# Kernel optimization log

Measured on AMD Instinct MI355X. Metric: run time of the kernel, lower is better.

## Reference

```python
import jax, jax.numpy as jnp
import numpy as np

N = 50000      # nodes
E = 800000     # edges (avg degree 16)
F = 32         # n_features
FOUT = 32      # n_features_out
L = 2          # n_layers (Message+Update pairs)
LEN = 10.0     # length_scale


def _mlp(x, w1, b1, w2, b2):
    # embedding.MLP: Linear -> SiLU -> Linear
    return jax.nn.silu(x @ w1 + b1) @ w2 + b2


def _posenc(d):
    # sinusoidal PositionalEncoder(F, length=LEN): ranks 1..F/2
    ranks = jnp.arange(1, F // 2 + 1, dtype=d.dtype)
    a = d[:, None] * ranks * (jnp.pi / LEN)           # [E, F/2]
    return jnp.concatenate([jnp.sin(a), jnp.cos(a)], axis=-1)  # [E, F]


def _painn(s, v, edge_index, edge_dist, edge_dir,
           mp_w1, mp_b1, mp_w2, mp_b2, mw_w1, mw_b1, mw_w2, mw_b2,
           u_U, u_V, u_w1, u_b1, u_w2, u_b2,
           ro_w1, ro_b1, ro_w2, ro_b2, ro_V):
    src, dst = edge_index[0], edge_index[1]
    pe = _posenc(edge_dist)                            # [E, F]
    dirb = edge_dir[:, None, :]                        # [E, 1, 3]
    for l in range(L):
        # ---- Message ----
        mix = _mlp(s[src], mp_w1[l], mp_b1[l], mp_w2[l], mp_b2[l]) \
            * _mlp(pe, mw_w1[l], mw_b1[l], mw_w2[l], mw_b2[l])     # [E, 4F]
        gates, cpg, sed, sf = jnp.split(mix, 4, axis=-1)
        cross = jnp.cross(dirb, v[dst])                # [E, F, 3] (broadcast)
        dv = sed[:, :, None] * dirb + gates[:, :, None] * v[src] \
           + cpg[:, :, None] * cross                   # [E, F, 3]
        ds = sf * s[src]                               # [E, F]
        v = v + jax.ops.segment_sum(dv, dst, num_segments=N)
        s = s + jax.ops.segment_sum(ds, dst, num_segments=N)
        # ---- Update ----
        Vv = jnp.einsum('nfc,fg->ngc', v, u_V[l])      # [N, F, 3]
        Uv = jnp.einsum('nfc,fg->ngc', v, u_U[l])
        Vn = jnp.linalg.norm(Vv, axis=-1)              # [N, F]
        g, ssn, add = jnp.split(
            _mlp(jnp.concatenate([Vn, s], axis=-1), u_w1[l], u_b1[l], u_w2[l], u_b2[l]),
            3, axis=-1)
        v = v + g[:, :, None] * Uv
        s = s + Vn * Vn * ssn + add
    # ---- Readout ----
    inv_out, gates = jnp.split(_mlp(s, ro_w1, ro_b1, ro_w2, ro_b2), 2, axis=-1)
    eqv_out = gates[:, :, None] * jnp.einsum('nfc,fg->ngc', v, ro_V)
    return inv_out, eqv_out


def setup_inputs() -> dict:
    key = jax.random.key(0)
    ks = iter(jax.random.split(key, 64))
    nk = lambda: next(ks)
    lin = lambda fin, fout, *lead: (jax.random.normal(nk(), (*lead, fin, fout), jnp.float32)
                                    / np.sqrt(fin).astype(np.float32))
    d = {}
    d['invariant_node_features'] = jax.random.normal(nk(), (N, F), jnp.float32)
    d['equivariant_node_features'] = jax.random.normal(nk(), (N, F, 3), jnp.float32)
    d['edge_index'] = jax.random.randint(nk(), (2, E), 0, N)
    d['edge_dist'] = jax.random.uniform(nk(), (E,), jnp.float32) * LEN
    g = jax.random.normal(nk(), (E, 3), jnp.float32)
    d['edge_dir'] = g / jnp.linalg.norm(g, axis=-1, keepdims=True)
    # Message MLPs (phi on node features, W on positional encoding)
    d['mp_w1'] = lin(F, F, L); d['mp_b1'] = jnp.zeros((L, F), jnp.float32)
    d['mp_w2'] = lin(F, 4 * F, L); d['mp_b2'] = jnp.zeros((L, 4 * F), jnp.float32)
    d['mw_w1'] = lin(F, F, L); d['mw_b1'] = jnp.zeros((L, F), jnp.float32)
    d['mw_w2'] = lin(F, 4 * F, L); d['mw_b2'] = jnp.zeros((L, 4 * F), jnp.float32)
    # Update: EquivariantLinear U, V and MLP(2F -> F -> 3F)
    d['u_U'] = lin(F, F, L); d['u_V'] = lin(F, F, L)
    d['u_w1'] = lin(2 * F, F, L); d['u_b1'] = jnp.zeros((L, F), jnp.float32)
    d['u_w2'] = lin(F, 3 * F, L); d['u_b2'] = jnp.zeros((L, 3 * F), jnp.float32)
    # Readout: MLP(F -> F -> 2*FOUT) and EquivariantLinear V (F -> FOUT)
    d['ro_w1'] = lin(F, F); d['ro_b1'] = jnp.zeros((F,), jnp.float32)
    d['ro_w2'] = lin(F, 2 * FOUT); d['ro_b2'] = jnp.zeros((2 * FOUT,), jnp.float32)
    d['ro_V'] = lin(F, FOUT)
    return d


def reference(invariant_node_features, equivariant_node_features, edge_index,
              edge_dist, edge_dir,
              mp_w1, mp_b1, mp_w2, mp_b2, mw_w1, mw_b1, mw_w2, mw_b2,
              u_U, u_V, u_w1, u_b1, u_w2, u_b2,
              ro_w1, ro_b1, ro_w2, ro_b2, ro_V):
    return _painn(invariant_node_features, equivariant_node_features, edge_index,
                  edge_dist, edge_dir,
                  mp_w1, mp_b1, mp_w2, mp_b2, mw_w1, mw_b1, mw_w2, mw_b2,
                  u_U, u_V, u_w1, u_b1, u_w2, u_b2,
                  ro_w1, ro_b1, ro_w2, ro_b2, ro_V)
```

## Files before the change

### kernel.cpp

```cpp
#include <hip/hip_runtime.h>
#include <math.h>

#define PI_LEN 0.3141592653589793f
#define LEN_F  10.0f
#define TBL    4096

__device__ __forceinline__ float fsilu(float x) {
  return x * __builtin_amdgcn_rcpf(1.f + __expf(-x));
}

__global__ __launch_bounds__(256) void hist_kernel(const int* __restrict__ ei,
                                                   int* __restrict__ deg, int E_) {
  int e = blockIdx.x * 256 + threadIdx.x;
  if (e < E_) atomicAdd(&deg[ei[E_ + e]], 1);
}

__global__ __launch_bounds__(1024) void scan_kernel(const int* __restrict__ deg,
                                                    int* __restrict__ off,
                                                    int* __restrict__ cursor, int N_) {
  __shared__ int wtot[16];
  __shared__ int carry_s;
  int tid = threadIdx.x, lane = tid & 63, wid = tid >> 6;
  if (tid == 0) carry_s = 0;
  __syncthreads();
  int nch = (N_ + 8191) / 8192;
  for (int c = 0; c < nch; ++c) {
    int base_idx = c * 8192 + tid * 8;
    int x[8]; int mysum = 0;
    #pragma unroll
    for (int j = 0; j < 8; ++j) { int idx = base_idx + j; x[j] = (idx < N_) ? deg[idx] : 0; mysum += x[j]; }
    int incl = mysum;
    #pragma unroll
    for (int s = 1; s < 64; s <<= 1) { int t = __shfl_up(incl, s, 64); if (lane >= s) incl += t; }
    if (lane == 63) wtot[wid] = incl;
    __syncthreads();
    if (wid == 0) {
      int wt = (lane < 16) ? wtot[lane] : 0;
      #pragma unroll
      for (int s = 1; s < 16; s <<= 1) { int t = __shfl_up(wt, s, 64); if (lane >= s) wt += t; }
      if (lane < 16) wtot[lane] = wt;
    }
    __syncthreads();
    int wexcl = (wid > 0) ? wtot[wid - 1] : 0;
    int run = carry_s + wexcl + (incl - mysum);
    #pragma unroll
    for (int j = 0; j < 8; ++j) {
      int idx = base_idx + j;
      if (idx < N_) { off[idx] = run; cursor[idx] = run; }
      run += x[j];
    }
    __syncthreads();
    if (tid == 0) carry_s += wtot[15];
    __syncthreads();
  }
  if (tid == 0) off[N_] = carry_s;
}

__global__ __launch_bounds__(256) void scatter_kernel(
    const int* __restrict__ ei, const float* __restrict__ dist,
    const float* __restrict__ edir, int* __restrict__ cursor,
    int* __restrict__ srcp, float4* __restrict__ edata, int E_) {
  int e = blockIdx.x * 256 + threadIdx.x;
  if (e < E_) {
    int dst = ei[E_ + e];
    int pos = atomicAdd(&cursor[dst], 1);
    srcp[pos] = ei[e];
    edata[pos] = make_float4(edir[3*e], edir[3*e+1], edir[3*e+2], dist[e]);
  }
}

__global__ __launch_bounds__(256) void nodeA_kernel(
    const float* __restrict__ s, const float* __restrict__ w1,
    const float* __restrict__ b1, const float* __restrict__ w2,
    const float* __restrict__ b2, float4* __restrict__ Aout4, int N_)
{
  __shared__ float xld[8][32];
  __shared__ float hld[8][32];
  int tid = threadIdx.x, i = tid >> 5, g = tid & 31;
  long n = (long)blockIdx.x * 8 + i;
  bool ok = (n < N_);
  xld[i][g] = ok ? s[n*32 + g] : 0.f;
  __syncthreads();
  float acc = b1[g];
  for (int k = 0; k < 32; ++k) acc += xld[i][k] * w1[k*32 + g];
  hld[i][g] = fsilu(acc);
  __syncthreads();
  float o0 = b2[g], o1 = b2[32+g], o2 = b2[64+g], o3 = b2[96+g];
  for (int k = 0; k < 32; ++k) {
    float hk = hld[i][k];
    o0 += hk * w2[k*128 +      g];
    o1 += hk * w2[k*128 + 32 + g];
    o2 += hk * w2[k*128 + 64 + g];
    o3 += hk * w2[k*128 + 96 + g];
  }
  if (ok) Aout4[n*32 + g] = make_float4(o0, o1, o2, o3 * xld[i][g]);
}

__global__ __launch_bounds__(256) void tbl_kernel(
    const float* __restrict__ w1, const float* __restrict__ b1,
    const float* __restrict__ w2, const float* __restrict__ b2,
    float4* __restrict__ tbl4)
{
  __shared__ float peld[8][32];
  __shared__ float hld[8][32];
  int tid = threadIdx.x, i = tid >> 5, g = tid & 31;
  int t = blockIdx.x * 8 + i;
  bool okt = (t <= TBL);
  float d = (float)t * (LEN_F / (float)TBL);
  float pe = (g < 16) ? __sinf(d * (float)(g + 1) * PI_LEN)
                      : __cosf(d * (float)(g - 15) * PI_LEN);
  peld[i][g] = pe;
  __syncthreads();
  float h = b1[g];
  for (int k = 0; k < 32; ++k) h += peld[i][k] * w1[k*32 + g];
  hld[i][g] = fsilu(h);
  __syncthreads();
  float o0 = b2[g], o1 = b2[32+g], o2 = b2[64+g], o3 = b2[96+g];
  for (int k = 0; k < 32; ++k) {
    float hk = hld[i][k];
    o0 += hk * w2[k*128 +      g];
    o1 += hk * w2[k*128 + 32 + g];
    o2 += hk * w2[k*128 + 64 + g];
    o3 += hk * w2[k*128 + 96 + g];
  }
  if (okt) tbl4[(long)t*32 + g] = make_float4(o0, o1, o2, o3);
}

#define EDGE_MATH(ED, M0, M1, FR, Av, V0, V1, V2)                         \
  {                                                                        \
    float ga = M0.x + FR*(M1.x - M0.x);                                    \
    float ca = M0.y + FR*(M1.y - M0.y);                                    \
    float da = M0.z + FR*(M1.z - M0.z);                                    \
    float sa = M0.w + FR*(M1.w - M0.w);                                    \
    float gates = ga*Av.x, cpg = ca*Av.y, sed = da*Av.z;                   \
    acc_s += sa*Av.w;                                                      \
    float crx = ED.y*vd2 - ED.z*vd1;                                       \
    float cry = ED.z*vd0 - ED.x*vd2;                                       \
    float crz = ED.x*vd1 - ED.y*vd0;                                       \
    av0 += sed*ED.x + gates*V0 + cpg*crx;                                  \
    av1 += sed*ED.y + gates*V1 + cpg*cry;                                  \
    av2 += sed*ED.z + gates*V2 + cpg*crz;                                  \
  }

__global__ __launch_bounds__(256) void gather_kernel(
    const int* __restrict__ off, const int* __restrict__ srcp,
    const float4* __restrict__ edata, const float4* __restrict__ tbl4,
    const float* __restrict__ v_prev, const float4* __restrict__ Aout4,
    float4* __restrict__ acc4, int N_)
{
  int tid = threadIdx.x, w = tid >> 6, lane = tid & 63, g = lane & 31, hf = lane >> 5;
  int n = blockIdx.x * 4 + w;
  if (n >= N_) return;
  const float* vp = v_prev + (long)n*96 + g*3;
  float vd0 = vp[0], vd1 = vp[1], vd2 = vp[2];
  int pstart = off[n], pend = off[n + 1];
  float acc_s = 0, av0 = 0, av1 = 0, av2 = 0;
  const float inv_step = (float)TBL / LEN_F;

  int deg = pend - pstart;
  int nfull = deg >> 3;
  int pb = pstart + hf * 4;
  for (int it = 0; it < nfull; ++it, pb += 8) {
    int srcs[4]; float4 ed[4];
    #pragma unroll
    for (int b = 0; b < 4; ++b) { srcs[b] = srcp[pb + b]; ed[b] = edata[pb + b]; }
    float4 m0[4], m1[4], A[4]; float fr[4];
    float vs0[4], vs1[4], vs2[4];
    #pragma unroll
    for (int b = 0; b < 4; ++b) {
      float x = ed[b].w * inv_step;
      float f = floorf(x);
      int i0 = (int)f; if (i0 > TBL - 1) i0 = TBL - 1;
      fr[b] = x - f;
      m0[b] = tbl4[(long)i0*32 + g];
      m1[b] = tbl4[(long)(i0 + 1)*32 + g];
      A[b]  = Aout4[(long)srcs[b]*32 + g];
      const float* vq = v_prev + (long)srcs[b]*96 + g*3;
      vs0[b] = vq[0]; vs1[b] = vq[1]; vs2[b] = vq[2];
    }
    #pragma unroll
    for (int b = 0; b < 4; ++b)
      EDGE_MATH(ed[b], m0[b], m1[b], fr[b], A[b], vs0[b], vs1[b], vs2[b]);
  }
  int p = pstart + nfull * 8 + hf;
  for (; p + 2 < pend; p += 4) {
    int  s0_ = srcp[p], s1_ = srcp[p + 2];
    float4 e0 = edata[p], e1 = edata[p + 2];
    float x0 = e0.w * inv_step, x1 = e1.w * inv_step;
    float f0 = floorf(x0), f1 = floorf(x1);
    int i0 = (int)f0; if (i0 > TBL - 1) i0 = TBL - 1;
    int i1 = (int)f1; if (i1 > TBL - 1) i1 = TBL - 1;
    float r0 = x0 - f0, r1 = x1 - f1;
    float4 a0 = tbl4[(long)i0*32 + g], b0 = tbl4[(long)(i0+1)*32 + g];
    float4 a1 = tbl4[(long)i1*32 + g], b1 = tbl4[(long)(i1+1)*32 + g];
    float4 A0 = Aout4[(long)s0_*32 + g], A1 = Aout4[(long)s1_*32 + g];
    const float* vq0 = v_prev + (long)s0_*96 + g*3;
    const float* vq1 = v_prev + (long)s1_*96 + g*3;
    float u0 = vq0[0], u1 = vq0[1], u2 = vq0[2];
    float t0 = vq1[0], t1 = vq1[1], t2 = vq1[2];
    EDGE_MATH(e0, a0, b0, r0, A0, u0, u1, u2);
    EDGE_MATH(e1, a1, b1, r1, A1, t0, t1, t2);
  }
  if (p < pend) {
    int  s0_ = srcp[p];
    float4 e0 = edata[p];
    float x0 = e0.w * inv_step;
    float f0 = floorf(x0);
    int i0 = (int)f0; if (i0 > TBL - 1) i0 = TBL - 1;
    float r0 = x0 - f0;
    float4 a0 = tbl4[(long)i0*32 + g], b0 = tbl4[(long)(i0+1)*32 + g];
    float4 A0 = Aout4[(long)s0_*32 + g];
    const float* vq0 = v_prev + (long)s0_*96 + g*3;
    float u0 = vq0[0], u1 = vq0[1], u2 = vq0[2];
    EDGE_MATH(e0, a0, b0, r0, A0, u0, u1, u2);
  }
  av0   += __shfl_xor(av0, 32);
  av1   += __shfl_xor(av1, 32);
  av2   += __shfl_xor(av2, 32);
  acc_s += __shfl_xor(acc_s, 32);
  if (hf == 0) acc4[(long)n*32 + g] = make_float4(av0, av1, av2, acc_s);
}

__global__ __launch_bounds__(256) void update_kernel(
    const float* __restrict__ s_prev, const float* __restrict__ v_prev,
    const float4* __restrict__ acc4,
    const float* __restrict__ uU, const float* __restrict__ uV,
    const float* __restrict__ uw1, const float* __restrict__ ub1,
    const float* __restrict__ uw2, const float* __restrict__ ub2,
    float* __restrict__ s_out, float* __restrict__ v_out, int N_)
{
  __shared__ float vld[8][96];
  __shared__ float in64[8][64];
  __shared__ float hld[8][32];
  int tid = threadIdx.x, i = tid >> 5, g = tid & 31;
  long n = (long)blockIdx.x * 8 + i;
  bool ok = (n < N_);
  float nv0 = 0, nv1 = 0, nv2 = 0, ns = 0;
  if (ok) {
    float4 a = acc4[n*32 + g];
    const float* vp = v_prev + n*96 + g*3;
    nv0 = vp[0] + a.x; nv1 = vp[1] + a.y; nv2 = vp[2] + a.z;
    ns  = s_prev[n*32 + g] + a.w;
  }
  vld[i][g*3+0] = nv0; vld[i][g*3+1] = nv1; vld[i][g*3+2] = nv2;
  __syncthreads();
  float Vv0=0,Vv1=0,Vv2=0,Uv0=0,Uv1=0,Uv2=0;
  for (int f = 0; f < 32; ++f) {
    float wu = uU[f*32 + g];
    float wv = uV[f*32 + g];
    float v0 = vld[i][f*3+0], v1 = vld[i][f*3+1], v2 = vld[i][f*3+2];
    Vv0 += v0*wv; Vv1 += v1*wv; Vv2 += v2*wv;
    Uv0 += v0*wu; Uv1 += v1*wu; Uv2 += v2*wu;
  }
  float Vn = sqrtf(Vv0*Vv0 + Vv1*Vv1 + Vv2*Vv2);
  in64[i][g] = Vn; in64[i][32 + g] = ns;
  __syncthreads();
  float h = ub1[g];
  for (int k = 0; k < 64; ++k) h += in64[i][k] * uw1[k*32 + g];
  h = fsilu(h);
  hld[i][g] = h;
  __syncthreads();
  float og = ub2[g], ossn = ub2[32 + g], oadd = ub2[64 + g];
  for (int k = 0; k < 32; ++k) {
    float hk = hld[i][k];
    og   += hk * uw2[k*96 +      g];
    ossn += hk * uw2[k*96 + 32 + g];
    oadd += hk * uw2[k*96 + 64 + g];
  }
  if (ok) {
    float* vo = v_out + n*96 + g*3;
    vo[0] = nv0 + og*Uv0;
    vo[1] = nv1 + og*Uv1;
    vo[2] = nv2 + og*Uv2;
    s_out[n*32 + g] = ns + Vn*Vn*ossn + oadd;
  }
}

__global__ __launch_bounds__(256) void readout_kernel(
    const float* __restrict__ s_cur, const float* __restrict__ v_cur,
    const float* __restrict__ w1, const float* __restrict__ b1,
    const float* __restrict__ w2, const float* __restrict__ b2,
    const float* __restrict__ roV, float* __restrict__ out, int N_)
{
  __shared__ float sld[8][32];
  __shared__ float hld[8][32];
  __shared__ float vld[8][96];
  int tid = threadIdx.x, i = tid >> 5, g = tid & 31;
  long n = (long)blockIdx.x * 8 + i;
  bool ok = (n < N_);
  if (ok) {
    sld[i][g] = s_cur[n*32 + g];
    const float* vp = v_cur + n*96 + g*3;
    vld[i][g*3+0] = vp[0]; vld[i][g*3+1] = vp[1]; vld[i][g*3+2] = vp[2];
  } else {
    sld[i][g] = 0.f;
    vld[i][g*3+0] = vld[i][g*3+1] = vld[i][g*3+2] = 0.f;
  }
  __syncthreads();
  float h = b1[g];
  for (int k = 0; k < 32; ++k) h += sld[i][k] * w1[k*32 + g];
  h = fsilu(h);
  hld[i][g] = h;
  __syncthreads();
  float inv = b2[g], gate = b2[32+g];
  for (int k = 0; k < 32; ++k) {
    float hk = hld[i][k];
    inv  += hk * w2[k*64 +      g];
    gate += hk * w2[k*64 + 32 + g];
  }
  float R0=0, R1=0, R2=0;
  for (int f = 0; f < 32; ++f) {
    float wv = roV[f*32 + g];
    R0 += vld[i][f*3+0]*wv; R1 += vld[i][f*3+1]*wv; R2 += vld[i][f*3+2]*wv;
  }
  if (ok) {
    out[n*32 + g] = inv;
    long eb = (long)N_*32 + n*96 + (long)g*3;
    out[eb+0] = gate*R0; out[eb+1] = gate*R1; out[eb+2] = gate*R2;
  }
}

extern "C" void kernel_launch(void* const* d_in, const int* in_sizes, int n_in,
                              void* d_out, int out_size, void* d_ws, size_t ws_size,
                              hipStream_t stream)
{
  const float* s_in  = (const float*)d_in[0];
  const float* v_in  = (const float*)d_in[1];
  const int*   ei    = (const int*)  d_in[2];
  const float* dist  = (const float*)d_in[3];
  const float* edir  = (const float*)d_in[4];
  const float* mp_w1 = (const float*)d_in[5];
  const float* mp_b1 = (const float*)d_in[6];
  const float* mp_w2 = (const float*)d_in[7];
  const float* mp_b2 = (const float*)d_in[8];
  const float* mw_w1 = (const float*)d_in[9];
  const float* mw_b1 = (const float*)d_in[10];
  const float* mw_w2 = (const float*)d_in[11];
  const float* mw_b2 = (const float*)d_in[12];
  const float* u_U   = (const float*)d_in[13];
  const float* u_V   = (const float*)d_in[14];
  const float* u_w1  = (const float*)d_in[15];
  const float* u_b1  = (const float*)d_in[16];
  const float* u_w2  = (const float*)d_in[17];
  const float* u_b2  = (const float*)d_in[18];
  const float* ro_w1 = (const float*)d_in[19];
  const float* ro_b1 = (const float*)d_in[20];
  const float* ro_w2 = (const float*)d_in[21];
  const float* ro_b2 = (const float*)d_in[22];
  const float* ro_V  = (const float*)d_in[23];

  int N_ = in_sizes[0] / 32;
  int E_ = in_sizes[3];

  float*  sA    = (float*)d_ws;
  float*  vA    = sA + (size_t)N_*32;
  float*  sB    = vA + (size_t)N_*96;
  float*  vB    = sB + (size_t)N_*32;
  float4* Aout4 = (float4*)(vB + (size_t)N_*96);
  float4* tbl4  = Aout4 + (size_t)N_*32;
  float4* edata = tbl4 + (size_t)(TBL+1)*32;
  int*    srcp  = (int*)(edata + (size_t)E_);
  int*    deg   = srcp + E_;
  int*    off   = deg + N_;
  int*    cursor= off + N_ + 1;

  float4* acc4  = (float4*)d_out;

  int nodeBlocks  = (N_ + 7) / 8;
  int gathBlocks  = (N_ + 3) / 4;
  int edgeBlocks  = (E_ + 255) / 256;
  int tblBlocks   = (TBL + 1 + 7) / 8;

  hipMemsetAsync(deg, 0, (size_t)N_ * sizeof(int), stream);
  hist_kernel<<<edgeBlocks, 256, 0, stream>>>(ei, deg, E_);
  scan_kernel<<<1, 1024, 0, stream>>>(deg, off, cursor, N_);
  scatter_kernel<<<edgeBlocks, 256, 0, stream>>>(ei, dist, edir, cursor, srcp, edata, E_);

  const float* s_cur = s_in;  const float* v_cur = v_in;
  float* s_nxt = sB;  float* v_nxt = vB;
  for (int l = 0; l < 2; ++l) {
    nodeA_kernel<<<nodeBlocks, 256, 0, stream>>>(
        s_cur, mp_w1 + l*1024, mp_b1 + l*32, mp_w2 + l*4096, mp_b2 + l*128, Aout4, N_);
    tbl_kernel<<<tblBlocks, 256, 0, stream>>>(
        mw_w1 + l*1024, mw_b1 + l*32, mw_w2 + l*4096, mw_b2 + l*128, tbl4);
    gather_kernel<<<gathBlocks, 256, 0, stream>>>(
        off, srcp, edata, tbl4, v_cur, Aout4, acc4, N_);
    update_kernel<<<nodeBlocks, 256, 0, stream>>>(
        s_cur, v_cur, acc4,
        u_U + l*1024, u_V + l*1024, u_w1 + l*2048, u_b1 + l*32,
        u_w2 + l*3072, u_b2 + l*96,
        s_nxt, v_nxt, N_);
    s_cur = s_nxt; v_cur = v_nxt;
    s_nxt = sA;    v_nxt = vA;
  }

  readout_kernel<<<nodeBlocks, 256, 0, stream>>>(
      s_cur, v_cur, ro_w1, ro_b1, ro_w2, ro_b2, ro_V, (float*)d_out, N_);
}
```

Before: 688.9 us.

## Fuse node MLP, table build, update and readout stages; widen masked gather loop

```diff
diff --git a/kernel.cpp b/kernel.cpp
--- a/kernel.cpp
+++ b/kernel.cpp
@@ -69,69 +69,70 @@
   }
 }
 
-__global__ __launch_bounds__(256) void nodeA_kernel(
-    const float* __restrict__ s, const float* __restrict__ w1,
-    const float* __restrict__ b1, const float* __restrict__ w2,
-    const float* __restrict__ b2, float4* __restrict__ Aout4, int N_)
-{
-  __shared__ float xld[8][32];
-  __shared__ float hld[8][32];
-  int tid = threadIdx.x, i = tid >> 5, g = tid & 31;
-  long n = (long)blockIdx.x * 8 + i;
-  bool ok = (n < N_);
-  xld[i][g] = ok ? s[n*32 + g] : 0.f;
-  __syncthreads();
-  float acc = b1[g];
-  for (int k = 0; k < 32; ++k) acc += xld[i][k] * w1[k*32 + g];
-  hld[i][g] = fsilu(acc);
-  __syncthreads();
+__device__ __forceinline__ void mlp_tbl_block(
+    int i, int g, int t,
+    const float* __restrict__ w1, const float* __restrict__ b1,
+    const float* __restrict__ w2, const float* __restrict__ b2,
+    float4* __restrict__ tbl4, float (*pe)[96], float (*hl)[32])
+{
+  bool okt = (t <= TBL);
+  float d = (float)t * (LEN_F / (float)TBL);
+  pe[i][g] = (g < 16) ? __sinf(d * (float)(g + 1) * PI_LEN)
+                      : __cosf(d * (float)(g - 15) * PI_LEN);
+  float h = b1[g];
+  for (int k = 0; k < 32; ++k) h += pe[i][k] * w1[k*32 + g];
+  hl[i][g] = fsilu(h);
   float o0 = b2[g], o1 = b2[32+g], o2 = b2[64+g], o3 = b2[96+g];
   for (int k = 0; k < 32; ++k) {
-    float hk = hld[i][k];
+    float hk = hl[i][k];
     o0 += hk * w2[k*128 +      g];
     o1 += hk * w2[k*128 + 32 + g];
     o2 += hk * w2[k*128 + 64 + g];
     o3 += hk * w2[k*128 + 96 + g];
   }
-  if (ok) Aout4[n*32 + g] = make_float4(o0, o1, o2, o3 * xld[i][g]);
-}
-
-__global__ __launch_bounds__(256) void tbl_kernel(
-    const float* __restrict__ w1, const float* __restrict__ b1,
-    const float* __restrict__ w2, const float* __restrict__ b2,
-    float4* __restrict__ tbl4)
-{
-  __shared__ float peld[8][32];
-  __shared__ float hld[8][32];
+  if (okt) tbl4[(long)t*32 + g] = make_float4(o0, o1, o2, o3);
+}
+
+__global__ __launch_bounds__(256) void nodeA_tbl_kernel(
+    const float* __restrict__ s,
+    const float* __restrict__ mpw1, const float* __restrict__ mpb1,
+    const float* __restrict__ mpw2, const float* __restrict__ mpb2,
+    const float* __restrict__ mww1, const float* __restrict__ mwb1,
+    const float* __restrict__ mww2, const float* __restrict__ mwb2,
+    float4* __restrict__ Aout4, float4* __restrict__ tbl4,
+    int N_, int nodeBlocks)
+{
+  __shared__ float a[8][96];
+  __shared__ float c[8][32];
   int tid = threadIdx.x, i = tid >> 5, g = tid & 31;
-  int t = blockIdx.x * 8 + i;
-  bool okt = (t <= TBL);
-  float d = (float)t * (LEN_F / (float)TBL);
-  float pe = (g < 16) ? __sinf(d * (float)(g + 1) * PI_LEN)
-                      : __cosf(d * (float)(g - 15) * PI_LEN);
-  peld[i][g] = pe;
-  __syncthreads();
-  float h = b1[g];
-  for (int k = 0; k < 32; ++k) h += peld[i][k] * w1[k*32 + g];
-  hld[i][g] = fsilu(h);
-  __syncthreads();
-  float o0 = b2[g], o1 = b2[32+g], o2 = b2[64+g], o3 = b2[96+g];
-  for (int k = 0; k < 32; ++k) {
-    float hk = hld[i][k];
-    o0 += hk * w2[k*128 +      g];
-    o1 += hk * w2[k*128 + 32 + g];
-    o2 += hk * w2[k*128 + 64 + g];
-    o3 += hk * w2[k*128 + 96 + g];
-  }
-  if (okt) tbl4[(long)t*32 + g] = make_float4(o0, o1, o2, o3);
-}
-
-#define EDGE_MATH(ED, M0, M1, FR, Av, V0, V1, V2)                         \
+  if (blockIdx.x >= nodeBlocks) {
+    int t = (blockIdx.x - nodeBlocks) * 8 + i;
+    mlp_tbl_block(i, g, t, mww1, mwb1, mww2, mwb2, tbl4, a, c);
+    return;
+  }
+  long n = (long)blockIdx.x * 8 + i;
+  bool ok = (n < N_);
+  a[i][g] = ok ? s[n*32 + g] : 0.f;
+  float h = mpb1[g];
+  for (int k = 0; k < 32; ++k) h += a[i][k] * mpw1[k*32 + g];
+  c[i][g] = fsilu(h);
+  float o0 = mpb2[g], o1 = mpb2[32+g], o2 = mpb2[64+g], o3 = mpb2[96+g];
+  for (int k = 0; k < 32; ++k) {
+    float hk = c[i][k];
+    o0 += hk * mpw2[k*128 +      g];
+    o1 += hk * mpw2[k*128 + 32 + g];
+    o2 += hk * mpw2[k*128 + 64 + g];
+    o3 += hk * mpw2[k*128 + 96 + g];
+  }
+  if (ok) Aout4[n*32 + g] = make_float4(o0, o1, o2, o3 * a[i][g]);
+}
+
+#define EDGE_MATH_M(ED, M0, M1, FR, MS, Av, V0, V1, V2)                    \
   {                                                                        \
-    float ga = M0.x + FR*(M1.x - M0.x);                                    \
-    float ca = M0.y + FR*(M1.y - M0.y);                                    \
-    float da = M0.z + FR*(M1.z - M0.z);                                    \
-    float sa = M0.w + FR*(M1.w - M0.w);                                    \
+    float ga = (M0.x + FR*(M1.x - M0.x)) * MS;                             \
+    float ca = (M0.y + FR*(M1.y - M0.y)) * MS;                             \
+    float da = (M0.z + FR*(M1.z - M0.z)) * MS;                             \
+    float sa = (M0.w + FR*(M1.w - M0.w)) * MS;                             \
     float gates = ga*Av.x, cpg = ca*Av.y, sed = da*Av.z;                   \
     acc_s += sa*Av.w;                                                      \
     float crx = ED.y*vd2 - ED.z*vd1;                                       \
@@ -157,62 +158,34 @@
   float acc_s = 0, av0 = 0, av1 = 0, av2 = 0;
   const float inv_step = (float)TBL / LEN_F;
 
-  int deg = pend - pstart;
-  int nfull = deg >> 3;
-  int pb = pstart + hf * 4;
-  for (int it = 0; it < nfull; ++it, pb += 8) {
-    int srcs[4]; float4 ed[4];
-    #pragma unroll
-    for (int b = 0; b < 4; ++b) { srcs[b] = srcp[pb + b]; ed[b] = edata[pb + b]; }
-    float4 m0[4], m1[4], A[4]; float fr[4];
-    float vs0[4], vs1[4], vs2[4];
-    #pragma unroll
-    for (int b = 0; b < 4; ++b) {
+  for (int p0 = pstart + hf * 8; p0 < pend; p0 += 16) {
+    int cnt = pend - p0; if (cnt > 8) cnt = 8;
+    int idx[8]; float4 ed[8];
+    #pragma unroll
+    for (int b = 0; b < 8; ++b) {
+      int p = (b < cnt) ? p0 + b : p0;
+      idx[b] = srcp[p];
+      ed[b]  = edata[p];
+    }
+    float4 m0[8], m1[8], A[8]; float fr[8];
+    float vs0[8], vs1[8], vs2[8];
+    #pragma unroll
+    for (int b = 0; b < 8; ++b) {
       float x = ed[b].w * inv_step;
       float f = floorf(x);
       int i0 = (int)f; if (i0 > TBL - 1) i0 = TBL - 1;
       fr[b] = x - f;
       m0[b] = tbl4[(long)i0*32 + g];
       m1[b] = tbl4[(long)(i0 + 1)*32 + g];
-      A[b]  = Aout4[(long)srcs[b]*32 + g];
-      const float* vq = v_prev + (long)srcs[b]*96 + g*3;
+      A[b]  = Aout4[(long)idx[b]*32 + g];
+      const float* vq = v_prev + (long)idx[b]*96 + g*3;
       vs0[b] = vq[0]; vs1[b] = vq[1]; vs2[b] = vq[2];
     }
     #pragma unroll
-    for (int b = 0; b < 4; ++b)
-      EDGE_MATH(ed[b], m0[b], m1[b], fr[b], A[b], vs0[b], vs1[b], vs2[b]);
-  }
-  int p = pstart + nfull * 8 + hf;
-  for (; p + 2 < pend; p += 4) {
-    int  s0_ = srcp[p], s1_ = srcp[p + 2];
-    float4 e0 = edata[p], e1 = edata[p + 2];
-    float x0 = e0.w * inv_step, x1 = e1.w * inv_step;
-    float f0 = floorf(x0), f1 = floorf(x1);
-    int i0 = (int)f0; if (i0 > TBL - 1) i0 = TBL - 1;
-    int i1 = (int)f1; if (i1 > TBL - 1) i1 = TBL - 1;
-    float r0 = x0 - f0, r1 = x1 - f1;
-    float4 a0 = tbl4[(long)i0*32 + g], b0 = tbl4[(long)(i0+1)*32 + g];
-    float4 a1 = tbl4[(long)i1*32 + g], b1 = tbl4[(long)(i1+1)*32 + g];
-    float4 A0 = Aout4[(long)s0_*32 + g], A1 = Aout4[(long)s1_*32 + g];
-    const float* vq0 = v_prev + (long)s0_*96 + g*3;
-    const float* vq1 = v_prev + (long)s1_*96 + g*3;
-    float u0 = vq0[0], u1 = vq0[1], u2 = vq0[2];
-    float t0 = vq1[0], t1 = vq1[1], t2 = vq1[2];
-    EDGE_MATH(e0, a0, b0, r0, A0, u0, u1, u2);
-    EDGE_MATH(e1, a1, b1, r1, A1, t0, t1, t2);
-  }
-  if (p < pend) {
-    int  s0_ = srcp[p];
-    float4 e0 = edata[p];
-    float x0 = e0.w * inv_step;
-    float f0 = floorf(x0);
-    int i0 = (int)f0; if (i0 > TBL - 1) i0 = TBL - 1;
-    float r0 = x0 - f0;
-    float4 a0 = tbl4[(long)i0*32 + g], b0 = tbl4[(long)(i0+1)*32 + g];
-    float4 A0 = Aout4[(long)s0_*32 + g];
-    const float* vq0 = v_prev + (long)s0_*96 + g*3;
-    float u0 = vq0[0], u1 = vq0[1], u2 = vq0[2];
-    EDGE_MATH(e0, a0, b0, r0, A0, u0, u1, u2);
+    for (int b = 0; b < 8; ++b) {
+      float msk = (b < cnt) ? 1.f : 0.f;
+      EDGE_MATH_M(ed[b], m0[b], m1[b], fr[b], msk, A[b], vs0[b], vs1[b], vs2[b]);
+    }
   }
   av0   += __shfl_xor(av0, 32);
   av1   += __shfl_xor(av1, 32);
@@ -221,13 +194,93 @@
   if (hf == 0) acc4[(long)n*32 + g] = make_float4(av0, av1, av2, acc_s);
 }
 
-__global__ __launch_bounds__(256) void update_kernel(
+__global__ __launch_bounds__(256) void update_mid_kernel(
     const float* __restrict__ s_prev, const float* __restrict__ v_prev,
     const float4* __restrict__ acc4,
     const float* __restrict__ uU, const float* __restrict__ uV,
     const float* __restrict__ uw1, const float* __restrict__ ub1,
     const float* __restrict__ uw2, const float* __restrict__ ub2,
-    float* __restrict__ s_out, float* __restrict__ v_out, int N_)
+    const float* __restrict__ nw1, const float* __restrict__ nb1,
+    const float* __restrict__ nw2, const float* __restrict__ nb2,
+    const float* __restrict__ tw1, const float* __restrict__ tb1,
+    const float* __restrict__ tw2, const float* __restrict__ tb2,
+    float* __restrict__ s_out, float* __restrict__ v_out,
+    float4* __restrict__ Aout4, float4* __restrict__ tbl4,
+    int N_, int nodeBlocks)
+{
+  __shared__ float vld[8][96];
+  __shared__ float in64[8][64];
+  __shared__ float hld[8][32];
+  int tid = threadIdx.x, i = tid >> 5, g = tid & 31;
+  if (blockIdx.x >= nodeBlocks) {
+    int t = (blockIdx.x - nodeBlocks) * 8 + i;
+    mlp_tbl_block(i, g, t, tw1, tb1, tw2, tb2, tbl4, vld, hld);
+    return;
+  }
+  long n = (long)blockIdx.x * 8 + i;
+  bool ok = (n < N_);
+  float nv0 = 0, nv1 = 0, nv2 = 0, ns = 0;
+  if (ok) {
+    float4 a = acc4[n*32 + g];
+    const float* vp = v_prev + n*96 + g*3;
+    nv0 = vp[0] + a.x; nv1 = vp[1] + a.y; nv2 = vp[2] + a.z;
+    ns  = s_prev[n*32 + g] + a.w;
+  }
+  vld[i][g*3+0] = nv0; vld[i][g*3+1] = nv1; vld[i][g*3+2] = nv2;
+  float Vv0=0,Vv1=0,Vv2=0,Uv0=0,Uv1=0,Uv2=0;
+  for (int f = 0; f < 32; ++f) {
+    float wu = uU[f*32 + g];
+    float wv = uV[f*32 + g];
+    float v0 = vld[i][f*3+0], v1 = vld[i][f*3+1], v2 = vld[i][f*3+2];
+    Vv0 += v0*wv; Vv1 += v1*wv; Vv2 += v2*wv;
+    Uv0 += v0*wu; Uv1 += v1*wu; Uv2 += v2*wu;
+  }
+  float Vn = sqrtf(Vv0*Vv0 + Vv1*Vv1 + Vv2*Vv2);
+  in64[i][g] = Vn; in64[i][32 + g] = ns;
+  float h = ub1[g];
+  for (int k = 0; k < 64; ++k) h += in64[i][k] * uw1[k*32 + g];
+  h = fsilu(h);
+  hld[i][g] = h;
+  float og = ub2[g], ossn = ub2[32 + g], oadd = ub2[64 + g];
+  for (int k = 0; k < 32; ++k) {
+    float hk = hld[i][k];
+    og   += hk * uw2[k*96 +      g];
+    ossn += hk * uw2[k*96 + 32 + g];
+    oadd += hk * uw2[k*96 + 64 + g];
+  }
+  float s_fin = ns + Vn*Vn*ossn + oadd;
+  if (ok) {
+    float* vo = v_out + n*96 + g*3;
+    vo[0] = nv0 + og*Uv0;
+    vo[1] = nv1 + og*Uv1;
+    vo[2] = nv2 + og*Uv2;
+    s_out[n*32 + g] = s_fin;
+  }
+  in64[i][g] = s_fin;
+  float h2 = nb1[g];
+  for (int k = 0; k < 32; ++k) h2 += in64[i][k] * nw1[k*32 + g];
+  h2 = fsilu(h2);
+  hld[i][g] = h2;
+  float o0 = nb2[g], o1 = nb2[32+g], o2 = nb2[64+g], o3 = nb2[96+g];
+  for (int k = 0; k < 32; ++k) {
+    float hk = hld[i][k];
+    o0 += hk * nw2[k*128 +      g];
+    o1 += hk * nw2[k*128 + 32 + g];
+    o2 += hk * nw2[k*128 + 64 + g];
+    o3 += hk * nw2[k*128 + 96 + g];
+  }
+  if (ok) Aout4[n*32 + g] = make_float4(o0, o1, o2, o3 * s_fin);
+}
+
+__global__ __launch_bounds__(256) void update_final_kernel(
+    const float* __restrict__ s_prev, const float* __restrict__ v_prev,
+    const float4* __restrict__ acc4,
+    const float* __restrict__ uU, const float* __restrict__ uV,
+    const float* __restrict__ uw1, const float* __restrict__ ub1,
+    const float* __restrict__ uw2, const float* __restrict__ ub2,
+    const float* __restrict__ rw1, const float* __restrict__ rb1,
+    const float* __restrict__ rw2, const float* __restrict__ rb2,
+    const float* __restrict__ roV, float* __restrict__ out, int N_)
 {
   __shared__ float vld[8][96];
   __shared__ float in64[8][64];
@@ -243,7 +296,6 @@
     ns  = s_prev[n*32 + g] + a.w;
   }
   vld[i][g*3+0] = nv0; vld[i][g*3+1] = nv1; vld[i][g*3+2] = nv2;
-  __syncthreads();
   float Vv0=0,Vv1=0,Vv2=0,Uv0=0,Uv1=0,Uv2=0;
   for (int f = 0; f < 32; ++f) {
     float wu = uU[f*32 + g];
@@ -254,12 +306,10 @@
   }
   float Vn = sqrtf(Vv0*Vv0 + Vv1*Vv1 + Vv2*Vv2);
   in64[i][g] = Vn; in64[i][32 + g] = ns;
-  __syncthreads();
   float h = ub1[g];
   for (int k = 0; k < 64; ++k) h += in64[i][k] * uw1[k*32 + g];
   h = fsilu(h);
   hld[i][g] = h;
-  __syncthreads();
   float og = ub2[g], ossn = ub2[32 + g], oadd = ub2[64 + g];
   for (int k = 0; k < 32; ++k) {
     float hk = hld[i][k];
@@ -267,48 +317,21 @@
     ossn += hk * uw2[k*96 + 32 + g];
     oadd += hk * uw2[k*96 + 64 + g];
   }
-  if (ok) {
-    float* vo = v_out + n*96 + g*3;
-    vo[0] = nv0 + og*Uv0;
-    vo[1] = nv1 + og*Uv1;
-    vo[2] = nv2 + og*Uv2;
-    s_out[n*32 + g] = ns + Vn*Vn*ossn + oadd;
-  }
-}
-
-__global__ __launch_bounds__(256) void readout_kernel(
-    const float* __restrict__ s_cur, const float* __restrict__ v_cur,
-    const float* __restrict__ w1, const float* __restrict__ b1,
-    const float* __restrict__ w2, const float* __restrict__ b2,
-    const float* __restrict__ roV, float* __restrict__ out, int N_)
-{
-  __shared__ float sld[8][32];
-  __shared__ float hld[8][32];
-  __shared__ float vld[8][96];
-  int tid = threadIdx.x, i = tid >> 5, g = tid & 31;
-  long n = (long)blockIdx.x * 8 + i;
-  bool ok = (n < N_);
-  if (ok) {
-    sld[i][g] = s_cur[n*32 + g];
-    const float* vp = v_cur + n*96 + g*3;
-    vld[i][g*3+0] = vp[0]; vld[i][g*3+1] = vp[1]; vld[i][g*3+2] = vp[2];
-  } else {
-    sld[i][g] = 0.f;
-    vld[i][g*3+0] = vld[i][g*3+1] = vld[i][g*3+2] = 0.f;
-  }
-  __syncthreads();
-  float h = b1[g];
-  for (int k = 0; k < 32; ++k) h += sld[i][k] * w1[k*32 + g];
-  h = fsilu(h);
-  hld[i][g] = h;
-  __syncthreads();
-  float inv = b2[g], gate = b2[32+g];
+  float s_fin = ns + Vn*Vn*ossn + oadd;
+  float vf0 = nv0 + og*Uv0, vf1 = nv1 + og*Uv1, vf2 = nv2 + og*Uv2;
+  in64[i][g] = s_fin;
+  float h2 = rb1[g];
+  for (int k = 0; k < 32; ++k) h2 += in64[i][k] * rw1[k*32 + g];
+  h2 = fsilu(h2);
+  hld[i][g] = h2;
+  float inv = rb2[g], gate = rb2[32 + g];
   for (int k = 0; k < 32; ++k) {
     float hk = hld[i][k];
-    inv  += hk * w2[k*64 +      g];
-    gate += hk * w2[k*64 + 32 + g];
-  }
-  float R0=0, R1=0, R2=0;
+    inv  += hk * rw2[k*64 +      g];
+    gate += hk * rw2[k*64 + 32 + g];
+  }
+  vld[i][g*3+0] = vf0; vld[i][g*3+1] = vf1; vld[i][g*3+2] = vf2;
+  float R0 = 0, R1 = 0, R2 = 0;
   for (int f = 0; f < 32; ++f) {
     float wv = roV[f*32 + g];
     R0 += vld[i][f*3+0]*wv; R1 += vld[i][f*3+1]*wv; R2 += vld[i][f*3+2]*wv;
@@ -352,48 +375,48 @@
   int N_ = in_sizes[0] / 32;
   int E_ = in_sizes[3];
 
-  float*  sA    = (float*)d_ws;
-  float*  vA    = sA + (size_t)N_*32;
-  float*  sB    = vA + (size_t)N_*96;
+  float*  sB    = (float*)d_ws;
   float*  vB    = sB + (size_t)N_*32;
   float4* Aout4 = (float4*)(vB + (size_t)N_*96);
-  float4* tbl4  = Aout4 + (size_t)N_*32;
+  float4* acc4b = Aout4 + (size_t)N_*32;
+  float4* tbl4  = acc4b + (size_t)N_*32;
   float4* edata = tbl4 + (size_t)(TBL+1)*32;
   int*    srcp  = (int*)(edata + (size_t)E_);
   int*    deg   = srcp + E_;
   int*    off   = deg + N_;
   int*    cursor= off + N_ + 1;
 
-  float4* acc4  = (float4*)d_out;
-
-  int nodeBlocks  = (N_ + 7) / 8;
-  int gathBlocks  = (N_ + 3) / 4;
-  int edgeBlocks  = (E_ + 255) / 256;
-  int tblBlocks   = (TBL + 1 + 7) / 8;
+  float4* acc4a = (float4*)d_out;
+
+  int nodeBlocks = (N_ + 7) / 8;
+  int gathBlocks = (N_ + 3) / 4;
+  int edgeBlocks = (E_ + 255) / 256;
+  int tblBlocks  = (TBL + 1 + 7) / 8;
 
   hipMemsetAsync(deg, 0, (size_t)N_ * sizeof(int), stream);
   hist_kernel<<<edgeBlocks, 256, 0, stream>>>(ei, deg, E_);
   scan_kernel<<<1, 1024, 0, stream>>>(deg, off, cursor, N_);
   scatter_kernel<<<edgeBlocks, 256, 0, stream>>>(ei, dist, edir, cursor, srcp, edata, E_);
 
-  const float* s_cur = s_in;  const float* v_cur = v_in;
-  float* s_nxt = sB;  float* v_nxt = vB;
-  for (int l = 0; l < 2; ++l) {
-    nodeA_kernel<<<nodeBlocks, 256, 0, stream>>>(
-        s_cur, mp_w1 + l*1024, mp_b1 + l*32, mp_w2 + l*4096, mp_b2 + l*128, Aout4, N_);
-    tbl_kernel<<<tblBlocks, 256, 0, stream>>>(
-        mw_w1 + l*1024, mw_b1 + l*32, mw_w2 + l*4096, mw_b2 + l*128, tbl4);
-    gather_kernel<<<gathBlocks, 256, 0, stream>>>(
-        off, srcp, edata, tbl4, v_cur, Aout4, acc4, N_);
-    update_kernel<<<nodeBlocks, 256, 0, stream>>>(
-        s_cur, v_cur, acc4,
-        u_U + l*1024, u_V + l*1024, u_w1 + l*2048, u_b1 + l*32,
-        u_w2 + l*3072, u_b2 + l*96,
-        s_nxt, v_nxt, N_);
-    s_cur = s_nxt; v_cur = v_nxt;
-    s_nxt = sA;    v_nxt = vA;
-  }
-
-  readout_kernel<<<nodeBlocks, 256, 0, stream>>>(
-      s_cur, v_cur, ro_w1, ro_b1, ro_w2, ro_b2, ro_V, (float*)d_out, N_);
-}
+  nodeA_tbl_kernel<<<nodeBlocks + tblBlocks, 256, 0, stream>>>(
+      s_in, mp_w1, mp_b1, mp_w2, mp_b2, mw_w1, mw_b1, mw_w2, mw_b2,
+      Aout4, tbl4, N_, nodeBlocks);
+
+  gather_kernel<<<gathBlocks, 256, 0, stream>>>(
+      off, srcp, edata, tbl4, v_in, Aout4, acc4a, N_);
+
+  update_mid_kernel<<<nodeBlocks + tblBlocks, 256, 0, stream>>>(
+      s_in, v_in, acc4a,
+      u_U, u_V, u_w1, u_b1, u_w2, u_b2,
+      mp_w1 + 1024, mp_b1 + 32, mp_w2 + 4096, mp_b2 + 128,
+      mw_w1 + 1024, mw_b1 + 32, mw_w2 + 4096, mw_b2 + 128,
+      sB, vB, Aout4, tbl4, N_, nodeBlocks);
+
+  gather_kernel<<<gathBlocks, 256, 0, stream>>>(
+      off, srcp, edata, tbl4, vB, Aout4, acc4b, N_);
+
+  update_final_kernel<<<nodeBlocks, 256, 0, stream>>>(
+      sB, vB, acc4b,
+      u_U + 1024, u_V + 1024, u_w1 + 2048, u_b1 + 32, u_w2 + 3072, u_b2 + 96,
+      ro_w1, ro_b1, ro_w2, ro_b2, ro_V, (float*)d_out, N_);
+}
```

Result: slower. 715.4 us (+3.8%).
